# Kernel tuning notes

Hardware: AMD Instinct MI355X
Metric: run time of the kernel (lower is better)

## Reference

```python
import jax, jax.numpy as jnp
import numpy as np

SIZE = 512
CHUNK = 16
NEG = -1e30  # stands in for -inf z key of invalid pixels
W_ATOL = 1e-8  # torch.isclose(w, 0) default atol


def setup_inputs() -> dict:
    key = jax.random.key(0)
    tris = jax.random.normal(key, (512, 3, 3), dtype=jnp.float32)  # [T,3,3] verts xyz in view space
    return {"tris": tris}


def _area2d(a, b, c):
    # (b.x - a.x)*(c.y - a.y) - (b.y - a.y)*(c.x - a.x); `a` may be batched [..., 2]
    return (b[0] - a[..., 0]) * (c[1] - a[..., 1]) - (b[1] - a[..., 1]) * (c[0] - a[..., 0])


def _tri_key_pts(tri, pts, xi, yi):
    """Per-triangle z key ([H,W], NEG where not covered) and interpolated 3d pts [H,W,3]."""
    t2 = tri[:, :2]
    w = _area2d(t2[0], t2[1], t2[2])  # signed parallelogram area, scalar
    pAB = _area2d(pts, t2[0], t2[1])
    pBC = _area2d(pts, t2[1], t2[2])
    pCA = _area2d(pts, t2[2], t2[0])
    inside = (pAB > 0) & (pBC > 0) & (pCA > 0)  # inside_mask: all sub-areas strictly positive
    # aabb clamped to [-1,1], converted to pixel indices with truncation (box2pts semantics)
    lo = jnp.clip(jnp.min(t2, axis=0), -1.0, 1.0)
    hi = jnp.clip(jnp.max(t2, axis=0), -1.0, 1.0)
    bb = ((jnp.concatenate([lo, hi]) + 1.0) * 0.5 * SIZE).astype(jnp.int32)
    inbox = (xi >= bb[0]) & (xi < bb[2]) & (yi >= bb[1]) & (yi < bb[3])
    valid_w = jnp.abs(w) > W_ATOL  # skip degenerate tri (torch.isclose(w, 0))
    sw = jnp.where(valid_w, w, 1.0)
    w1 = pAB / sw
    w2 = pBC / sw
    w3 = 1.0 - w1 - w2
    p3 = w1[..., None] * tri[0] + w2[..., None] * tri[1] + w3[..., None] * tri[2]  # [H,W,3]
    valid = inside & inbox & valid_w
    keyz = jnp.where(valid, p3[..., 2], jnp.asarray(NEG, p3.dtype))
    return keyz, p3


def _render(tris):
    T = tris.shape[0]
    lin = jnp.linspace(-1.0, 1.0, SIZE, dtype=tris.dtype)
    px, py = jnp.meshgrid(lin, lin, indexing="ij")  # lookup_table
    pts = jnp.stack([px, py], axis=-1)  # [H,W,2]
    xi, yi = jnp.meshgrid(jnp.arange(SIZE), jnp.arange(SIZE), indexing="ij")
    zmin = jnp.min(tris[..., 2])  # initial zbuffer value
    tris_c = tris.reshape(T // CHUNK, CHUNK, 3, 3)

    def step(carry, tchunk):
        zbuf, res = carry
        keyz, p3 = jax.vmap(_tri_key_pts, in_axes=(0, None, None, None))(tchunk, pts, xi, yi)
        idx = CHUNK - 1 - jnp.argmax(keyz[::-1], axis=0)  # last argmax in chunk
        bz = jnp.take_along_axis(keyz, idx[None], axis=0)[0]  # [H,W]
        bp = jnp.take_along_axis(p3, idx[None, ..., None], axis=0)[0]  # [H,W,3]
        upd = bz >= zbuf  # invalid pixels carry NEG and never pass
        zbuf = jnp.where(upd, bz, zbuf)
        new = jnp.concatenate([bp, jnp.ones_like(bp[..., :1])], axis=-1)  # rgb=pts3d, alpha=1
        res = jnp.where(upd[..., None], new, res)
        return (zbuf, res), None

    init = (jnp.full((SIZE, SIZE), zmin, dtype=tris.dtype), jnp.zeros((SIZE, SIZE, 4), dtype=tris.dtype))
    (zbuf, res), _ = jax.lax.scan(jax.checkpoint(step), init, tris_c)
    return res


def reference(tris):
    return _render(tris)
```

## Files before the change

kernel.cpp:

```cpp
#include <hip/hip_runtime.h>

#define SIZE 512
#define NTRI 512

#pragma clang fp contract(off)

__device__ __forceinline__ float lin_at(int i) {
    if (i == SIZE - 1) return 1.0f;
    float s = __fdiv_rn((float)i, 511.0f);
    float u = 1.0f - s;
    return s - u;
}

__device__ __forceinline__ float4 shade(const float* __restrict__ tris, int bi,
                                        float px, float py) {
#pragma clang fp contract(off)
    if (bi < 0) return make_float4(0.0f, 0.0f, 0.0f, 0.0f);
    const float* p = tris + bi * 9;
    float a0 = p[0], a1 = p[1], a2 = p[2];
    float b0 = p[3], b1 = p[4], b2 = p[5];
    float c0 = p[6], c1 = p[7], c2 = p[8];
    float w = (b0 - a0) * (c1 - a1) - (b1 - a1) * (c0 - a0);
    float sw = (fabsf(w) > 1e-8f) ? w : 1.0f;
    float dax = a0 - px, day = a1 - py;
    float dbx = b0 - px, dby = b1 - py;
    float dcx = c0 - px, dcy = c1 - py;
    float pAB = dax * dby - day * dbx;
    float pBC = dbx * dcy - dby * dcx;
    float w1 = __fdiv_rn(pAB, sw);
    float w2 = __fdiv_rn(pBC, sw);
    float w3 = 1.0f - w1 - w2;
    float x = (w1 * a0 + w2 * b0) + w3 * c0;
    float y = (w1 * a1 + w2 * b1) + w3 * c1;
    float z = (w1 * a2 + w2 * b2) + w3 * c2;
    return make_float4(x, y, z, 1.0f);
}

__global__ __launch_bounds__(256) void render_kernel(const float* __restrict__ tris,
                                                     float* __restrict__ out) {
#pragma clang fp contract(off)
    __shared__ float4 szp[NTRI];
    __shared__ int4   sbb[NTRI];
    __shared__ float4 sv0[NTRI];
    __shared__ float2 sv1[NTRI];
    __shared__ unsigned long long smA[8], smB[8], smC[8];
    __shared__ float sredz[4], sredm[4];

    const int tx = threadIdx.x;
    const int ty = threadIdx.y;
    const int tid = ty * 16 + tx;
    const int lane = tid & 63, wv = tid >> 6;
    const unsigned long long lt = (1ull << lane) - 1ull;

    const int i0 = blockIdx.y * 16;
    const int j0 = blockIdx.x * 16;

    const float pxlo = lin_at(i0), pxhi = lin_at(i0 + 15);
    const float pylo = lin_at(j0), pyhi = lin_at(j0 + 15);

    float va0[2], va1[2], vb0[2], vb1[2], vc0[2], vc1[2];
    float vzc[2], vzx[2], vzy[2], vtzx[2];
    int   vx0[2], vy0[2], vx1[2], vy1[2];
    bool  vIF[2], vIP[2], vEX[2];

    float zm = 1e30f;
    float mloc = -1e30f;
#pragma unroll
    for (int r = 0; r < 2; ++r) {
        const int t = tid + r * 256;
        const float* p = tris + t * 9;
        float a0 = p[0], a1 = p[1], a2 = p[2];
        float b0 = p[3], b1 = p[4], b2 = p[5];
        float c0 = p[6], c1 = p[7], c2 = p[8];
        va0[r] = a0; va1[r] = a1;
        vb0[r] = b0; vb1[r] = b1;
        vc0[r] = c0; vc1[r] = c1;

        zm = fminf(zm, fminf(a2, fminf(b2, c2)));

        float w = (b0 - a0) * (c1 - a1) - (b1 - a1) * (c0 - a0);
        bool vw = fabsf(w) > 1e-8f;
        float sw = vw ? w : 1.0f;

        float lox = fminf(fminf(a0, b0), c0);
        float loy = fminf(fminf(a1, b1), c1);
        float hix = fmaxf(fmaxf(a0, b0), c0);
        float hiy = fmaxf(fmaxf(a1, b1), c1);
        int bb0 = (int)((fminf(fmaxf(lox, -1.0f), 1.0f) + 1.0f) * 0.5f * 512.0f);
        int bb1 = (int)((fminf(fmaxf(loy, -1.0f), 1.0f) + 1.0f) * 0.5f * 512.0f);
        int bb2 = (int)((fminf(fmaxf(hix, -1.0f), 1.0f) + 1.0f) * 0.5f * 512.0f);
        int bb3 = (int)((fminf(fmaxf(hiy, -1.0f), 1.0f) + 1.0f) * 0.5f * 512.0f);
        vx0[r] = bb0; vy0[r] = bb1; vx1[r] = bb2; vy1[r] = bb3;

        bool cand = vw && (w > -1e-4f) &&
                    (bb0 < i0 + 16) && (bb2 > i0) &&
                    (bb1 < j0 + 16) && (bb3 > j0);

        float cAB = a0 * b1 - a1 * b0, gxAB = a1 - b1, gyAB = b0 - a0;
        float cBC = b0 * c1 - b1 * c0, gxBC = b1 - c1, gyBC = c0 - b0;
        float cCA = c0 * a1 - c1 * a0, gxCA = c1 - a1, gyCA = a0 - c0;

        bool allIn = false;
        if (cand) {
            float x0, x1, y0, y1, mx, mn;
            x0 = gxAB * pxlo; x1 = gxAB * pxhi; y0 = gyAB * pylo; y1 = gyAB * pyhi;
            mx = cAB + fmaxf(x0, x1) + fmaxf(y0, y1);
            mn = cAB + fminf(x0, x1) + fminf(y0, y1);
            cand = mx >= -1e-3f;
            allIn = mn > 1e-3f;
            x0 = gxBC * pxlo; x1 = gxBC * pxhi; y0 = gyBC * pylo; y1 = gyBC * pyhi;
            mx = cBC + fmaxf(x0, x1) + fmaxf(y0, y1);
            mn = cBC + fminf(x0, x1) + fminf(y0, y1);
            cand = cand && (mx >= -1e-3f);
            allIn = allIn && (mn > 1e-3f);
            x0 = gxCA * pxlo; x1 = gxCA * pxhi; y0 = gyCA * pylo; y1 = gyCA * pyhi;
            mx = cCA + fmaxf(x0, x1) + fmaxf(y0, y1);
            mn = cCA + fminf(x0, x1) + fminf(y0, y1);
            cand = cand && (mx >= -1e-3f);
            allIn = allIn && (mn > 1e-3f);
        }

        float rsw = __builtin_amdgcn_rcpf(sw);
        float k1 = (a2 - c2) * rsw;
        float k2 = (b2 - c2) * rsw;
        float zc = c2 + k1 * cAB + k2 * cBC;
        float zx = k1 * gxAB + k2 * gxBC;
        float zy = k1 * gyAB + k2 * gyBC;
        vzc[r] = zc; vzx[r] = zx; vzy[r] = zy;

        float zxl = zx * pxlo, zxh = zx * pxhi;
        float zyl = zy * pylo, zyh = zy * pyhi;
        float tzmin = zc + fminf(zxl, zxh) + fminf(zyl, zyh);
        float tzmax = zc + fmaxf(zxl, zxh) + fmaxf(zyl, zyh);
        vtzx[r] = tzmax;

        bool full = (bb0 <= i0) && (bb2 >= i0 + 16) &&
                    (bb1 <= j0) && (bb3 >= j0 + 16);
        vIF[r] = cand && allIn && full;
        vIP[r] = cand && allIn && !full;
        vEX[r] = cand && !allIn;

        if (vIF[r]) mloc = fmaxf(mloc, tzmin);
    }

    for (int off = 32; off; off >>= 1) {
        zm = fminf(zm, __shfl_xor(zm, off));
        mloc = fmaxf(mloc, __shfl_xor(mloc, off));
    }
    if (lane == 0) { sredz[wv] = zm; sredm[wv] = mloc; }
    __syncthreads();
    const float zmin = fminf(fminf(sredz[0], sredz[1]), fminf(sredz[2], sredz[3]));
    const float M = fmaxf(fmaxf(sredm[0], sredm[1]), fmaxf(sredm[2], sredm[3]));
    const float cullb = fmaxf(M, zmin) - 1e-4f;

#pragma unroll
    for (int r = 0; r < 2; ++r) {
        bool keep = vtzx[r] >= cullb;
        vIF[r] &= keep; vIP[r] &= keep; vEX[r] &= keep;
        unsigned long long mA = __ballot(vIF[r]);
        unsigned long long mB = __ballot(vIP[r]);
        unsigned long long mC = __ballot(vEX[r]);
        if (lane == 0) { smA[r * 4 + wv] = mA; smB[r * 4 + wv] = mB; smC[r * 4 + wv] = mC; }
    }
    __syncthreads();

    int bA[8], bB[8], bC[8], c = 0;
#pragma unroll
    for (int g = 0; g < 8; ++g) { bA[g] = c; c += __popcll(smA[g]); }
    const int cntA = c;
#pragma unroll
    for (int g = 0; g < 8; ++g) { bB[g] = c; c += __popcll(smB[g]); }
    const int cntB = c;
#pragma unroll
    for (int g = 0; g < 8; ++g) { bC[g] = c; c += __popcll(smC[g]); }
    const int cntC = c;

#pragma unroll
    for (int r = 0; r < 2; ++r) {
        if (vIF[r] || vIP[r] || vEX[r]) {
            const int g = r * 4 + wv;
            const int t = tid + r * 256;
            int pos;
            if (vIF[r])      pos = bA[g] + __popcll(smA[g] & lt);
            else if (vIP[r]) pos = bB[g] + __popcll(smB[g] & lt);
            else             pos = bC[g] + __popcll(smC[g] & lt);

            szp[pos] = make_float4(vzc[r], vzx[r], vzy[r], __int_as_float(t));
            if (!vIF[r]) sbb[pos] = make_int4(vx0[r], vy0[r], vx1[r], vy1[r]);
            if (vEX[r]) {
                sv0[pos] = make_float4(va0[r], va1[r], vb0[r], vb1[r]);
                sv1[pos] = make_float2(vc0[r], vc1[r]);
            }
        }
    }
    __syncthreads();

    const int j = j0 + tx;
    const int i = i0 + ty;
    const float px = lin_at(i);
    const float py = lin_at(j);

    float best = zmin;
    float bf = __int_as_float(-1);

#pragma unroll 4
    for (int k = 0; k < cntA; ++k) {
        float4 zp = szp[k];
        float z = fmaf(zp.y, px, fmaf(zp.z, py, zp.x));
        if (z >= best) { best = z; bf = zp.w; }
    }
#pragma unroll 4
    for (int k = cntA; k < cntB; ++k) {
        float4 zp = szp[k];
        int4 bb = sbb[k];
        float z = fmaf(zp.y, px, fmaf(zp.z, py, zp.x));
        bool in = (i >= bb.x) & (i < bb.z) & (j >= bb.y) & (j < bb.w);
        if (in & (z >= best)) { best = z; bf = zp.w; }
    }
#pragma unroll 2
    for (int k = cntB; k < cntC; ++k) {
        float4 zp = szp[k];
        float4 f0 = sv0[k];
        float2 f1 = sv1[k];
        int4 bb = sbb[k];
        float dax = f0.x - px, day = f0.y - py;
        float dbx = f0.z - px, dby = f0.w - py;
        float dcx = f1.x - px, dcy = f1.y - py;
        float pAB = dax * dby - day * dbx;
        float pBC = dbx * dcy - dby * dcx;
        float pCA = dcx * day - dcy * dax;
        bool cov = (pAB > 0.0f) & (pBC > 0.0f) & (pCA > 0.0f) &
                   (i >= bb.x) & (i < bb.z) & (j >= bb.y) & (j < bb.w);
        float z = fmaf(zp.y, px, fmaf(zp.z, py, zp.x));
        if (cov & (z >= best)) { best = z; bf = zp.w; }
    }

    ((float4*)out)[i * SIZE + j] = shade(tris, __float_as_int(bf), px, py);
}

extern "C" void kernel_launch(void* const* d_in, const int* in_sizes, int n_in,
                              void* d_out, int out_size, void* d_ws, size_t ws_size,
                              hipStream_t stream) {
    const float* tris = (const float*)d_in[0];
    float* out = (float*)d_out;
    dim3 grid(SIZE / 16, SIZE / 16, 1);
    dim3 block(16, 16, 1);
    render_kernel<<<grid, block, 0, stream>>>(tris, out);
}
```

Measured before the change: 12.45 us.

## Use 512-thread blocks, one triangle per thread, split candidate scan across two halves

The block grows from 256 to 512 threads, so each thread sets up exactly one triangle instead of looping over two. In the per-pixel phase two threads share each pixel and take alternate candidates, then their results are merged through shared memory with a later-index tie-break. The aim is to cut the serial triangle-setup and candidate-scan latency per block. The cost is an extra barrier and merge step, plus higher register pressure at 512 threads per block.

New measurement: 15.20 us. 1.22x slower.

```diff
diff --git a/kernel.cpp b/kernel.cpp
--- a/kernel.cpp
+++ b/kernel.cpp
@@ -36,19 +36,18 @@
     return make_float4(x, y, z, 1.0f);
 }
 
-__global__ __launch_bounds__(256) void render_kernel(const float* __restrict__ tris,
-                                                     float* __restrict__ out) {
+__global__ __launch_bounds__(512, 8) void render_kernel(const float* __restrict__ tris,
+                                                        float* __restrict__ out) {
 #pragma clang fp contract(off)
     __shared__ float4 szp[NTRI];
     __shared__ int4   sbb[NTRI];
     __shared__ float4 sv0[NTRI];
     __shared__ float2 sv1[NTRI];
     __shared__ unsigned long long smA[8], smB[8], smC[8];
-    __shared__ float sredz[4], sredm[4];
-
-    const int tx = threadIdx.x;
-    const int ty = threadIdx.y;
-    const int tid = ty * 16 + tx;
+    __shared__ float sredz[8], sredm[8];
+    __shared__ float2 smrg[256];
+
+    const int tid = threadIdx.x;
     const int lane = tid & 63, wv = tid >> 6;
     const unsigned long long lt = (1ull << lane) - 1ull;
 
@@ -58,90 +57,74 @@
     const float pxlo = lin_at(i0), pxhi = lin_at(i0 + 15);
     const float pylo = lin_at(j0), pyhi = lin_at(j0 + 15);
 
-    float va0[2], va1[2], vb0[2], vb1[2], vc0[2], vc1[2];
-    float vzc[2], vzx[2], vzy[2], vtzx[2];
-    int   vx0[2], vy0[2], vx1[2], vy1[2];
-    bool  vIF[2], vIP[2], vEX[2];
-
-    float zm = 1e30f;
-    float mloc = -1e30f;
-#pragma unroll
-    for (int r = 0; r < 2; ++r) {
-        const int t = tid + r * 256;
-        const float* p = tris + t * 9;
-        float a0 = p[0], a1 = p[1], a2 = p[2];
-        float b0 = p[3], b1 = p[4], b2 = p[5];
-        float c0 = p[6], c1 = p[7], c2 = p[8];
-        va0[r] = a0; va1[r] = a1;
-        vb0[r] = b0; vb1[r] = b1;
-        vc0[r] = c0; vc1[r] = c1;
-
-        zm = fminf(zm, fminf(a2, fminf(b2, c2)));
-
-        float w = (b0 - a0) * (c1 - a1) - (b1 - a1) * (c0 - a0);
-        bool vw = fabsf(w) > 1e-8f;
-        float sw = vw ? w : 1.0f;
-
-        float lox = fminf(fminf(a0, b0), c0);
-        float loy = fminf(fminf(a1, b1), c1);
-        float hix = fmaxf(fmaxf(a0, b0), c0);
-        float hiy = fmaxf(fmaxf(a1, b1), c1);
-        int bb0 = (int)((fminf(fmaxf(lox, -1.0f), 1.0f) + 1.0f) * 0.5f * 512.0f);
-        int bb1 = (int)((fminf(fmaxf(loy, -1.0f), 1.0f) + 1.0f) * 0.5f * 512.0f);
-        int bb2 = (int)((fminf(fmaxf(hix, -1.0f), 1.0f) + 1.0f) * 0.5f * 512.0f);
-        int bb3 = (int)((fminf(fmaxf(hiy, -1.0f), 1.0f) + 1.0f) * 0.5f * 512.0f);
-        vx0[r] = bb0; vy0[r] = bb1; vx1[r] = bb2; vy1[r] = bb3;
-
-        bool cand = vw && (w > -1e-4f) &&
-                    (bb0 < i0 + 16) && (bb2 > i0) &&
-                    (bb1 < j0 + 16) && (bb3 > j0);
-
-        float cAB = a0 * b1 - a1 * b0, gxAB = a1 - b1, gyAB = b0 - a0;
-        float cBC = b0 * c1 - b1 * c0, gxBC = b1 - c1, gyBC = c0 - b0;
-        float cCA = c0 * a1 - c1 * a0, gxCA = c1 - a1, gyCA = a0 - c0;
-
-        bool allIn = false;
-        if (cand) {
-            float x0, x1, y0, y1, mx, mn;
-            x0 = gxAB * pxlo; x1 = gxAB * pxhi; y0 = gyAB * pylo; y1 = gyAB * pyhi;
-            mx = cAB + fmaxf(x0, x1) + fmaxf(y0, y1);
-            mn = cAB + fminf(x0, x1) + fminf(y0, y1);
-            cand = mx >= -1e-3f;
-            allIn = mn > 1e-3f;
-            x0 = gxBC * pxlo; x1 = gxBC * pxhi; y0 = gyBC * pylo; y1 = gyBC * pyhi;
-            mx = cBC + fmaxf(x0, x1) + fmaxf(y0, y1);
-            mn = cBC + fminf(x0, x1) + fminf(y0, y1);
-            cand = cand && (mx >= -1e-3f);
-            allIn = allIn && (mn > 1e-3f);
-            x0 = gxCA * pxlo; x1 = gxCA * pxhi; y0 = gyCA * pylo; y1 = gyCA * pyhi;
-            mx = cCA + fmaxf(x0, x1) + fmaxf(y0, y1);
-            mn = cCA + fminf(x0, x1) + fminf(y0, y1);
-            cand = cand && (mx >= -1e-3f);
-            allIn = allIn && (mn > 1e-3f);
-        }
-
-        float rsw = __builtin_amdgcn_rcpf(sw);
-        float k1 = (a2 - c2) * rsw;
-        float k2 = (b2 - c2) * rsw;
-        float zc = c2 + k1 * cAB + k2 * cBC;
-        float zx = k1 * gxAB + k2 * gxBC;
-        float zy = k1 * gyAB + k2 * gyBC;
-        vzc[r] = zc; vzx[r] = zx; vzy[r] = zy;
-
-        float zxl = zx * pxlo, zxh = zx * pxhi;
-        float zyl = zy * pylo, zyh = zy * pyhi;
-        float tzmin = zc + fminf(zxl, zxh) + fminf(zyl, zyh);
-        float tzmax = zc + fmaxf(zxl, zxh) + fmaxf(zyl, zyh);
-        vtzx[r] = tzmax;
-
-        bool full = (bb0 <= i0) && (bb2 >= i0 + 16) &&
-                    (bb1 <= j0) && (bb3 >= j0 + 16);
-        vIF[r] = cand && allIn && full;
-        vIP[r] = cand && allIn && !full;
-        vEX[r] = cand && !allIn;
-
-        if (vIF[r]) mloc = fmaxf(mloc, tzmin);
-    }
+    const int t = tid;
+    const float* p = tris + t * 9;
+    float a0 = p[0], a1 = p[1], a2 = p[2];
+    float b0 = p[3], b1 = p[4], b2 = p[5];
+    float c0 = p[6], c1 = p[7], c2 = p[8];
+
+    float zm = fminf(a2, fminf(b2, c2));
+
+    float w = (b0 - a0) * (c1 - a1) - (b1 - a1) * (c0 - a0);
+    bool vw = fabsf(w) > 1e-8f;
+    float sw = vw ? w : 1.0f;
+
+    float lox = fminf(fminf(a0, b0), c0);
+    float loy = fminf(fminf(a1, b1), c1);
+    float hix = fmaxf(fmaxf(a0, b0), c0);
+    float hiy = fmaxf(fmaxf(a1, b1), c1);
+    int bb0 = (int)((fminf(fmaxf(lox, -1.0f), 1.0f) + 1.0f) * 0.5f * 512.0f);
+    int bb1 = (int)((fminf(fmaxf(loy, -1.0f), 1.0f) + 1.0f) * 0.5f * 512.0f);
+    int bb2 = (int)((fminf(fmaxf(hix, -1.0f), 1.0f) + 1.0f) * 0.5f * 512.0f);
+    int bb3 = (int)((fminf(fmaxf(hiy, -1.0f), 1.0f) + 1.0f) * 0.5f * 512.0f);
+
+    bool cand = vw && (w > -1e-4f) &&
+                (bb0 < i0 + 16) && (bb2 > i0) &&
+                (bb1 < j0 + 16) && (bb3 > j0);
+
+    float cAB = a0 * b1 - a1 * b0, gxAB = a1 - b1, gyAB = b0 - a0;
+    float cBC = b0 * c1 - b1 * c0, gxBC = b1 - c1, gyBC = c0 - b0;
+    float cCA = c0 * a1 - c1 * a0, gxCA = c1 - a1, gyCA = a0 - c0;
+
+    bool allIn = false;
+    if (cand) {
+        float x0, x1, y0, y1, mx, mn;
+        x0 = gxAB * pxlo; x1 = gxAB * pxhi; y0 = gyAB * pylo; y1 = gyAB * pyhi;
+        mx = cAB + fmaxf(x0, x1) + fmaxf(y0, y1);
+        mn = cAB + fminf(x0, x1) + fminf(y0, y1);
+        cand = mx >= -1e-3f;
+        allIn = mn > 1e-3f;
+        x0 = gxBC * pxlo; x1 = gxBC * pxhi; y0 = gyBC * pylo; y1 = gyBC * pyhi;
+        mx = cBC + fmaxf(x0, x1) + fmaxf(y0, y1);
+        mn = cBC + fminf(x0, x1) + fminf(y0, y1);
+        cand = cand && (mx >= -1e-3f);
+        allIn = allIn && (mn > 1e-3f);
+        x0 = gxCA * pxlo; x1 = gxCA * pxhi; y0 = gyCA * pylo; y1 = gyCA * pyhi;
+        mx = cCA + fmaxf(x0, x1) + fmaxf(y0, y1);
+        mn = cCA + fminf(x0, x1) + fminf(y0, y1);
+        cand = cand && (mx >= -1e-3f);
+        allIn = allIn && (mn > 1e-3f);
+    }
+
+    float rsw = __builtin_amdgcn_rcpf(sw);
+    float k1 = (a2 - c2) * rsw;
+    float k2 = (b2 - c2) * rsw;
+    float zc = c2 + k1 * cAB + k2 * cBC;
+    float zx = k1 * gxAB + k2 * gxBC;
+    float zy = k1 * gyAB + k2 * gyBC;
+
+    float zxl = zx * pxlo, zxh = zx * pxhi;
+    float zyl = zy * pylo, zyh = zy * pyhi;
+    float tzmin = zc + fminf(zxl, zxh) + fminf(zyl, zyh);
+    float tzmax = zc + fmaxf(zxl, zxh) + fmaxf(zyl, zyh);
+
+    bool full = (bb0 <= i0) && (bb2 >= i0 + 16) &&
+                (bb1 <= j0) && (bb3 >= j0 + 16);
+    bool vIF = cand && allIn && full;
+    bool vIP = cand && allIn && !full;
+    bool vEX = cand && !allIn;
+
+    float mloc = vIF ? tzmin : -1e30f;
 
     for (int off = 32; off; off >>= 1) {
         zm = fminf(zm, __shfl_xor(zm, off));
@@ -149,18 +132,18 @@
     }
     if (lane == 0) { sredz[wv] = zm; sredm[wv] = mloc; }
     __syncthreads();
-    const float zmin = fminf(fminf(sredz[0], sredz[1]), fminf(sredz[2], sredz[3]));
-    const float M = fmaxf(fmaxf(sredm[0], sredm[1]), fmaxf(sredm[2], sredm[3]));
+    float zmin = sredz[0], M = sredm[0];
+#pragma unroll
+    for (int g = 1; g < 8; ++g) { zmin = fminf(zmin, sredz[g]); M = fmaxf(M, sredm[g]); }
     const float cullb = fmaxf(M, zmin) - 1e-4f;
 
-#pragma unroll
-    for (int r = 0; r < 2; ++r) {
-        bool keep = vtzx[r] >= cullb;
-        vIF[r] &= keep; vIP[r] &= keep; vEX[r] &= keep;
-        unsigned long long mA = __ballot(vIF[r]);
-        unsigned long long mB = __ballot(vIP[r]);
-        unsigned long long mC = __ballot(vEX[r]);
-        if (lane == 0) { smA[r * 4 + wv] = mA; smB[r * 4 + wv] = mB; smC[r * 4 + wv] = mC; }
+    {
+        bool keep = tzmax >= cullb;
+        vIF &= keep; vIP &= keep; vEX &= keep;
+        unsigned long long mA = __ballot(vIF);
+        unsigned long long mB = __ballot(vIP);
+        unsigned long long mC = __ballot(vEX);
+        if (lane == 0) { smA[wv] = mA; smB[wv] = mB; smC[wv] = mC; }
     }
     __syncthreads();
 
@@ -175,50 +158,49 @@
     for (int g = 0; g < 8; ++g) { bC[g] = c; c += __popcll(smC[g]); }
     const int cntC = c;
 
-#pragma unroll
-    for (int r = 0; r < 2; ++r) {
-        if (vIF[r] || vIP[r] || vEX[r]) {
-            const int g = r * 4 + wv;
-            const int t = tid + r * 256;
-            int pos;
-            if (vIF[r])      pos = bA[g] + __popcll(smA[g] & lt);
-            else if (vIP[r]) pos = bB[g] + __popcll(smB[g] & lt);
-            else             pos = bC[g] + __popcll(smC[g] & lt);
-
-            szp[pos] = make_float4(vzc[r], vzx[r], vzy[r], __int_as_float(t));
-            if (!vIF[r]) sbb[pos] = make_int4(vx0[r], vy0[r], vx1[r], vy1[r]);
-            if (vEX[r]) {
-                sv0[pos] = make_float4(va0[r], va1[r], vb0[r], vb1[r]);
-                sv1[pos] = make_float2(vc0[r], vc1[r]);
-            }
+    if (vIF || vIP || vEX) {
+        int pos;
+        if (vIF)      pos = bA[wv] + __popcll(smA[wv] & lt);
+        else if (vIP) pos = bB[wv] + __popcll(smB[wv] & lt);
+        else          pos = bC[wv] + __popcll(smC[wv] & lt);
+
+        szp[pos] = make_float4(zc, zx, zy, __int_as_float(t));
+        if (!vIF) sbb[pos] = make_int4(bb0, bb1, bb2, bb3);
+        if (vEX) {
+            sv0[pos] = make_float4(a0, a1, b0, b1);
+            sv1[pos] = make_float2(c0, c1);
         }
     }
     __syncthreads();
 
+    const int pix = tid & 255;
+    const int h   = tid >> 8;
+    const int tx  = pix & 15;
+    const int tyq = pix >> 4;
     const int j = j0 + tx;
-    const int i = i0 + ty;
+    const int i = i0 + tyq;
     const float px = lin_at(i);
     const float py = lin_at(j);
 
     float best = zmin;
-    float bf = __int_as_float(-1);
+    int   bt = -1;
 
 #pragma unroll 4
-    for (int k = 0; k < cntA; ++k) {
+    for (int k = h; k < cntA; k += 2) {
         float4 zp = szp[k];
         float z = fmaf(zp.y, px, fmaf(zp.z, py, zp.x));
-        if (z >= best) { best = z; bf = zp.w; }
+        if (z >= best) { best = z; bt = __float_as_int(zp.w); }
     }
 #pragma unroll 4
-    for (int k = cntA; k < cntB; ++k) {
+    for (int k = cntA + h; k < cntB; k += 2) {
         float4 zp = szp[k];
         int4 bb = sbb[k];
         float z = fmaf(zp.y, px, fmaf(zp.z, py, zp.x));
         bool in = (i >= bb.x) & (i < bb.z) & (j >= bb.y) & (j < bb.w);
-        if (in & (z >= best)) { best = z; bf = zp.w; }
+        if (in & (z >= best)) { best = z; bt = __float_as_int(zp.w); }
     }
 #pragma unroll 2
-    for (int k = cntB; k < cntC; ++k) {
+    for (int k = cntB + h; k < cntC; k += 2) {
         float4 zp = szp[k];
         float4 f0 = sv0[k];
         float2 f1 = sv1[k];
@@ -232,10 +214,18 @@
         bool cov = (pAB > 0.0f) & (pBC > 0.0f) & (pCA > 0.0f) &
                    (i >= bb.x) & (i < bb.z) & (j >= bb.y) & (j < bb.w);
         float z = fmaf(zp.y, px, fmaf(zp.z, py, zp.x));
-        if (cov & (z >= best)) { best = z; bf = zp.w; }
-    }
-
-    ((float4*)out)[i * SIZE + j] = shade(tris, __float_as_int(bf), px, py);
+        if (cov & (z >= best)) { best = z; bt = __float_as_int(zp.w); }
+    }
+
+    if (h == 1) smrg[pix] = make_float2(best, __int_as_float(bt));
+    __syncthreads();
+    if (h == 0) {
+        float2 o = smrg[pix];
+        float zB = o.x;
+        int tB = __float_as_int(o.y);
+        if ((zB > best) | ((zB == best) & (tB > bt))) { best = zB; bt = tB; }
+        ((float4*)out)[i * SIZE + j] = shade(tris, bt, px, py);
+    }
 }
 
 extern "C" void kernel_launch(void* const* d_in, const int* in_sizes, int n_in,
@@ -244,6 +234,6 @@
     const float* tris = (const float*)d_in[0];
     float* out = (float*)d_out;
     dim3 grid(SIZE / 16, SIZE / 16, 1);
-    dim3 block(16, 16, 1);
+    dim3 block(512, 1, 1);
     render_kernel<<<grid, block, 0, stream>>>(tris, out);
 }
```
